# Optimization experiments

Hardware: AMD Instinct MI355X
Metric: run time of the kernel (lower is better)

Reference implementation:

```python
import jax, jax.numpy as jnp
import numpy as np

NUM_HEADS = 12
NUM_GROUPS = 4
LN_EPS = 1e-12
NEG = -10000.0


def _ln(x, g, b):
    m = x.mean(-1, keepdims=True)
    v = ((x - m) ** 2).mean(-1, keepdims=True)
    return (x - m) * jax.lax.rsqrt(v + LN_EPS) * g + b


def _attention(h, ext_mask, Wattn, battn, ln):
    # h: [B,S,H]; ext_mask additive [B,1,1,S]; Wattn [4,H,H] = (q,k,v,o); battn [4,H]; ln [2,H]
    B, S, H = h.shape
    dh = H // NUM_HEADS
    q = (h @ Wattn[0] + battn[0]).reshape(B, S, NUM_HEADS, dh)
    k = (h @ Wattn[1] + battn[1]).reshape(B, S, NUM_HEADS, dh)
    v = (h @ Wattn[2] + battn[2]).reshape(B, S, NUM_HEADS, dh)
    scores = jnp.einsum('bqhd,bkhd->bhqk', q, k) * (1.0 / np.sqrt(dh)) + ext_mask
    p = jax.nn.softmax(scores, axis=-1)
    ctx = jnp.einsum('bhqk,bkhd->bqhd', p, v).reshape(B, S, H)
    # BertSelfOutput: dense + residual + LayerNorm
    return _ln(ctx @ Wattn[3] + battn[3] + h, ln[0], ln[1])


def _ffn(x, Wi, bi, Wo, bo, ln):
    # BertIntermediate (gelu) + BertOutput (dense + residual + LayerNorm)
    return _ln(jax.nn.gelu(x @ Wi + bi, approximate=False) @ Wo + bo + x, ln[0], ln[1])


def _bert_layer(h, ext_mask, Wattn, battn, ln_attn, Wi, bi, Wo, bo, ln_out):
    a = _attention(h, ext_mask, Wattn, battn, ln_attn)
    return _ffn(a, Wi, bi, Wo, bo, ln_out)


def _hier_attention(h, hier_mask, Wattn, battn, ln_attn, Wi, bi, Wo, bo, ln_out):
    # group masks [G,B,S]: 1 where hier_mask == group_id (ids 1..G)
    gids = jnp.arange(1, NUM_GROUPS + 1)
    masks = (hier_mask[None] == gids[:, None, None]).astype(h.dtype)  # [G,B,S]
    ext = (1.0 - masks)[:, :, None, None, :] * NEG                    # [G,B,1,1,S]
    # one full BertLayer per group (vectorized over G instead of batch concat)
    outs = jax.vmap(lambda m: _bert_layer(h, m, Wattn, battn, ln_attn, Wi, bi, Wo, bo, ln_out))(ext)  # [G,B,S,H]
    return jnp.sum(outs * masks[..., None], axis=0)


def reference(hidden_states, attention_mask, main_Wattn, main_battn, main_ln_attn,
              main_Wi, main_bi, main_Wo, main_bo, main_ln_out,
              hier_Wattn, hier_battn, hier_ln_attn, hier_Wi, hier_bi, hier_Wo,
              hier_bo, hier_ln_out, hier_mask):
    attn_out = _attention(hidden_states, attention_mask, main_Wattn, main_battn, main_ln_attn)
    hier_out = _hier_attention(hidden_states, hier_mask, hier_Wattn, hier_battn,
                               hier_ln_attn, hier_Wi, hier_bi, hier_Wo, hier_bo, hier_ln_out)
    combined = attn_out + hier_out
    return _ffn(combined, main_Wi, main_bi, main_Wo, main_bo, main_ln_out)


def setup_inputs() -> dict:
    key = jax.random.key(0)
    ks = jax.random.split(key, 20)
    B, S, H, F = 8, 512, 768, 3072
    W = 0.02  # weight init scale

    def layer_params(k):
        kk = jax.random.split(k, 8)
        return dict(
            Wattn=jax.random.normal(kk[0], (4, H, H), jnp.float32) * W,
            battn=jax.random.normal(kk[1], (4, H), jnp.float32) * W,
            ln_attn=jnp.stack([1.0 + jax.random.normal(kk[2], (H,), jnp.float32) * W,
                               jax.random.normal(kk[3], (H,), jnp.float32) * W]),
            Wi=jax.random.normal(kk[4], (H, F), jnp.float32) * W,
            bi=jax.random.normal(kk[5], (F,), jnp.float32) * W,
            Wo=jax.random.normal(kk[6], (F, H), jnp.float32) * W,
            bo=jax.random.normal(kk[7], (H,), jnp.float32) * W,
            ln_out=jnp.stack([1.0 + jax.random.normal(kk[2], (H,), jnp.float32) * W,
                              jax.random.normal(kk[3], (H,), jnp.float32) * W]),
        )

    main = layer_params(ks[0])
    hier = layer_params(ks[1])
    inp = {
        'hidden_states': jax.random.normal(ks[2], (B, S, H), jnp.float32),
        'attention_mask': jnp.zeros((B, 1, 1, S), jnp.float32),
        'hier_mask': jax.random.randint(ks[3], (B, S), 0, 5).astype(jnp.int64),
    }
    for name, p in (('main', main), ('hier', hier)):
        for k2, v in p.items():
            inp[f'{name}_{k2}'] = v
    return inp
```

## Files before the change

kernel.cpp:

```cpp
#include <hip/hip_runtime.h>
#include <hip/hip_bf16.h>

#define DI __device__ __forceinline__

typedef __attribute__((ext_vector_type(4))) float  f32x4;
typedef __attribute__((ext_vector_type(8))) short  s16x8;
typedef __attribute__((ext_vector_type(4))) short  s16x4;
typedef __attribute__((ext_vector_type(8))) __bf16 bf16x8;

DI short f2bf(float f) {
  union { float f; unsigned u; } v; v.f = f;
  unsigned r = v.u + 0x7fffu + ((v.u >> 16) & 1u);
  return (short)(r >> 16);
}

DI f32x4 mfma16(s16x8 a, s16x8 b, f32x4 c) {
  return __builtin_amdgcn_mfma_f32_16x16x32_bf16(
      __builtin_bit_cast(bf16x8, a), __builtin_bit_cast(bf16x8, b), c, 0, 0, 0);
}

typedef const __attribute__((address_space(1))) unsigned* gas_p;
typedef __attribute__((address_space(3))) unsigned* las_p;
DI void gload16(const void* g, void* l) {
  __builtin_amdgcn_global_load_lds((gas_p)g, (las_p)l, 16, 0, 0);
}

__global__ __launch_bounds__(256) void cast_bf16(const float* __restrict__ x,
                                                 short* __restrict__ y) {
  const int i = (blockIdx.x * 256 + threadIdx.x) * 4;
  const float4 t = *(const float4*)&x[i];
  s16x4 o;
  o[0] = f2bf(t.x); o[1] = f2bf(t.y); o[2] = f2bf(t.z); o[3] = f2bf(t.w);
  *(s16x4*)&y[i] = o;
}

struct TJob { const float* src; short* dst; int K, N, tile0; };
struct TJobs { TJob j[12]; };

__global__ __launch_bounds__(256) void transpose_w(TJobs jobs) {
  __shared__ float T[32][33];
  const int t = blockIdx.x;
  int ji = 0;
#pragma unroll
  for (int i = 1; i < 12; ++i) if (jobs.j[i].tile0 <= t) ji = i;
  const float* src = jobs.j[ji].src;
  short* dst = jobs.j[ji].dst;
  const int K = jobs.j[ji].K, N = jobs.j[ji].N;
  const int lt = t - jobs.j[ji].tile0;
  const int tn = N >> 5;
  const int n0 = (lt % tn) << 5, k0 = (lt / tn) << 5;
  const int tid = threadIdx.x;
#pragma unroll
  for (int i = 0; i < 4; ++i) {
    const int c = i * 256 + tid, r = c >> 5, cc = c & 31;
    T[cc][r] = src[(long long)(k0 + r) * N + n0 + cc];
  }
  __syncthreads();
#pragma unroll
  for (int i = 0; i < 4; ++i) {
    const int c = i * 256 + tid, r = c >> 5, cc = c & 31;
    dst[(long long)(n0 + r) * K + k0 + cc] = f2bf(T[r][cc]);
  }
}

__global__ __launch_bounds__(256) void transpose_v(const short* __restrict__ QKV,
                                                   short* __restrict__ Vt) {
  __shared__ short T[64][72];
  const int bh = blockIdx.y;
  const int b = bh / 12, hh = bh % 12;
  const int s0 = blockIdx.x * 64;
  const int tid = threadIdx.x;
#pragma unroll
  for (int i = 0; i < 2; ++i) {
    const int c = i * 256 + tid;
    const int s = c >> 3, d = (c & 7) * 8;
    s16x8 v = *(const s16x8*)&QKV[(long long)(b * 512 + s0 + s) * 2304 + 1536 + hh * 64 + d];
    *(s16x8*)&T[s][d] = v;
  }
  __syncthreads();
#pragma unroll
  for (int i = 0; i < 2; ++i) {
    const int c = i * 256 + tid;
    const int d = c >> 3, s = (c & 7) * 8;
    s16x8 v;
#pragma unroll
    for (int j = 0; j < 8; ++j) v[j] = T[s + j][d];
    *(s16x8*)&Vt[(long long)bh * 32768 + (long long)d * 512 + s0 + s] = v;
  }
}

template<int BM, int BN, int WM, int WN, int EPI>
__global__ __launch_bounds__(256) void gemm_bt(
    const short* __restrict__ A, int lda, long long sA,
    const short* __restrict__ B, int ldb, long long sB,
    void* __restrict__ Cv, int ldc,
    long long cOuter, int cInner, int cStride,
    const float* __restrict__ bias,
    int K, int nSplit) {
  constexpr int BK = 32;
  constexpr int WNW = BN / WN;
  constexpr int MFR = WM / 16, NFR = WN / 16;
  constexpr int ACH = BM * 4;
  constexpr int BCH = BN * 4;

  __shared__ short As[BM * BK];
  __shared__ short Bs[BN * BK];

  const int z = blockIdx.z;
  const int zb = z / nSplit, zs = z - zb * nSplit;
  const short* Ab = A + (long long)zb * sA + (long long)zs * K;
  const short* Bb = B + (long long)zb * sB + (long long)zs * K;
  const long long cOff = (long long)(z / cInner) * cOuter + (long long)(z % cInner) * cStride;

  const int bm = blockIdx.x * BM;
  const int bn = blockIdx.y * BN;
  const int tid = threadIdx.x;
  const int wave = tid >> 6, lane = tid & 63;
  const int wm = (wave / WNW) * WM;
  const int wn = (wave % WNW) * WN;
  const int l16 = lane & 15, lk = lane >> 4;

  f32x4 acc[MFR][NFR] = {};

  for (int kt = 0; kt < K; kt += BK) {
    __syncthreads();
#pragma unroll
    for (int i = 0; i < ACH / 256; ++i) {
      const int c = i * 256 + tid;
      gload16(Ab + (long long)(bm + (c >> 2)) * lda + kt + (c & 3) * 8,
              &As[(i * 256 + wave * 64) * 8]);
    }
#pragma unroll
    for (int i = 0; i < BCH / 256; ++i) {
      const int c = i * 256 + tid;
      gload16(Bb + (long long)(bn + (c >> 2)) * ldb + kt + (c & 3) * 8,
              &Bs[(i * 256 + wave * 64) * 8]);
    }
    __syncthreads();
    s16x8 af[MFR], bfr[NFR];
#pragma unroll
    for (int mi = 0; mi < MFR; ++mi)
      af[mi] = *(const s16x8*)&As[(wm + mi * 16 + l16) * BK + lk * 8];
#pragma unroll
    for (int ni = 0; ni < NFR; ++ni)
      bfr[ni] = *(const s16x8*)&Bs[(wn + ni * 16 + l16) * BK + lk * 8];
#pragma unroll
    for (int mi = 0; mi < MFR; ++mi)
#pragma unroll
      for (int ni = 0; ni < NFR; ++ni)
        acc[mi][ni] = mfma16(af[mi], bfr[ni], acc[mi][ni]);
  }

#pragma unroll
  for (int ni = 0; ni < NFR; ++ni) {
    const int col = bn + wn + ni * 16 + l16;
    const float bv = (EPI != 2 && bias) ? bias[col] : 0.f;
#pragma unroll
    for (int mi = 0; mi < MFR; ++mi) {
#pragma unroll
      for (int r = 0; r < 4; ++r) {
        const int row = bm + wm + mi * 16 + lk * 4 + r;
        const long long idx = cOff + (long long)row * ldc + col;
        float v = acc[mi][ni][r] + bv;
        if constexpr (EPI == 0) {
          ((short*)Cv)[idx] = f2bf(v);
        } else if constexpr (EPI == 1) {
          v = 0.5f * v * (1.f + erff(v * 0.70710678118654752f));
          ((short*)Cv)[idx] = f2bf(v);
        } else {
          ((float*)Cv)[idx] = v;
        }
      }
    }
  }
}

template<int HIER>
__global__ __launch_bounds__(256) void attn_scores(
    const short* __restrict__ QKV,
    const float* __restrict__ amask,
    const int* __restrict__ hmask,
    short* __restrict__ P) {
  __shared__ short Qs[32 * 64];
  __shared__ short Ks[256 * 64];
  __shared__ float red[32 * 4];
  __shared__ int   hm[512];

  const int bh = blockIdx.y;
  const int b = bh / 12, hh = bh % 12;
  const int q0 = blockIdx.x * 32;
  const int tid = threadIdx.x;
  const int wave = tid >> 6, lane = tid & 63;
  const int l16 = lane & 15, lk = lane >> 4;
  const long long rowbase = (long long)(b * 512) * 2304 + hh * 64;

  {
    const int c = tid;
    gload16(QKV + rowbase + (long long)(q0 + (c >> 3)) * 2304 + (c & 7) * 8,
            &Qs[wave * 64 * 8]);
  }
  if constexpr (HIER) {
    for (int i = tid; i < 512; i += 256) hm[i] = hmask[b * 512 + i];
  }

  f32x4 acc[2][8] = {};
#pragma unroll
  for (int kc = 0; kc < 2; ++kc) {
    if (kc) __syncthreads();
#pragma unroll
    for (int i = 0; i < 8; ++i) {
      const int c = i * 256 + tid;
      gload16(QKV + rowbase + 768 + (long long)(kc * 256 + (c >> 3)) * 2304 + (c & 7) * 8,
              &Ks[(i * 256 + wave * 64) * 8]);
    }
    __syncthreads();
#pragma unroll
    for (int ks = 0; ks < 2; ++ks) {
      s16x8 af[2], bfr[4];
#pragma unroll
      for (int mi = 0; mi < 2; ++mi)
        af[mi] = *(const s16x8*)&Qs[(mi * 16 + l16) * 64 + ks * 32 + lk * 8];
#pragma unroll
      for (int ni = 0; ni < 4; ++ni)
        bfr[ni] = *(const s16x8*)&Ks[(wave * 64 + ni * 16 + l16) * 64 + ks * 32 + lk * 8];
#pragma unroll
      for (int mi = 0; mi < 2; ++mi)
#pragma unroll
        for (int ni = 0; ni < 4; ++ni)
          acc[mi][kc * 4 + ni] = mfma16(af[mi], bfr[ni], acc[mi][kc * 4 + ni]);
    }
  }

  int gq[2][4];
  if constexpr (HIER) {
#pragma unroll
    for (int mi = 0; mi < 2; ++mi)
#pragma unroll
      for (int r = 0; r < 4; ++r)
        gq[mi][r] = hm[q0 + mi * 16 + lk * 4 + r];
  }
  int hk[8]; float am[8];
#pragma unroll
  for (int nig = 0; nig < 8; ++nig) {
    const int col = (nig >> 2) * 256 + wave * 64 + (nig & 3) * 16 + l16;
    if constexpr (HIER) hk[nig] = hm[col];
    else                am[nig] = amask[b * 512 + col];
  }
#pragma unroll
  for (int mi = 0; mi < 2; ++mi)
#pragma unroll
    for (int nig = 0; nig < 8; ++nig)
#pragma unroll
      for (int r = 0; r < 4; ++r) {
        float v = acc[mi][nig][r] * 0.125f;
        if constexpr (HIER) v += (hk[nig] == gq[mi][r]) ? 0.f : -10000.f;
        else                v += am[nig];
        acc[mi][nig][r] = v;
      }

  float mx[2][4];
#pragma unroll
  for (int mi = 0; mi < 2; ++mi)
#pragma unroll
    for (int r = 0; r < 4; ++r) {
      float m = acc[mi][0][r];
#pragma unroll
      for (int nig = 1; nig < 8; ++nig) m = fmaxf(m, acc[mi][nig][r]);
#pragma unroll
      for (int d = 1; d < 16; d <<= 1) m = fmaxf(m, __shfl_xor(m, d));
      mx[mi][r] = m;
      red[(mi * 16 + lk * 4 + r) * 4 + wave] = m;
    }
  __syncthreads();
#pragma unroll
  for (int mi = 0; mi < 2; ++mi)
#pragma unroll
    for (int r = 0; r < 4; ++r) {
      const int q = mi * 16 + lk * 4 + r;
      mx[mi][r] = fmaxf(fmaxf(red[q * 4], red[q * 4 + 1]),
                        fmaxf(red[q * 4 + 2], red[q * 4 + 3]));
    }
  __syncthreads();

  float sm[2][4];
#pragma unroll
  for (int mi = 0; mi < 2; ++mi)
#pragma unroll
    for (int r = 0; r < 4; ++r) {
      float s = 0.f;
#pragma unroll
      for (int nig = 0; nig < 8; ++nig) {
        const float e = __expf(acc[mi][nig][r] - mx[mi][r]);
        acc[mi][nig][r] = e;
        s += e;
      }
#pragma unroll
      for (int d = 1; d < 16; d <<= 1) s += __shfl_xor(s, d);
      sm[mi][r] = s;
      red[(mi * 16 + lk * 4 + r) * 4 + wave] = s;
    }
  __syncthreads();
#pragma unroll
  for (int mi = 0; mi < 2; ++mi)
#pragma unroll
    for (int r = 0; r < 4; ++r) {
      const int q = mi * 16 + lk * 4 + r;
      sm[mi][r] = 1.f / (red[q * 4] + red[q * 4 + 1] + red[q * 4 + 2] + red[q * 4 + 3]);
    }

  const long long Pbase = (long long)bh * 512 * 512;
#pragma unroll
  for (int mi = 0; mi < 2; ++mi)
#pragma unroll
    for (int nig = 0; nig < 8; ++nig) {
      const int col = (nig >> 2) * 256 + wave * 64 + (nig & 3) * 16 + l16;
#pragma unroll
      for (int r = 0; r < 4; ++r) {
        const int q = mi * 16 + lk * 4 + r;
        P[Pbase + (long long)(q0 + q) * 512 + col] = f2bf(acc[mi][nig][r] * sm[mi][r]);
      }
    }
}

template<int NS, int MODE>
__global__ __launch_bounds__(256) void ln_red(
    const float* __restrict__ part, const float* __restrict__ bias,
    const float* __restrict__ res, const float* __restrict__ ln,
    float* __restrict__ outf, short* __restrict__ outb,
    const int* __restrict__ hmask) {
  constexpr long long SP = 4096LL * 768;
  const int row = blockIdx.x * 4 + (threadIdx.x >> 6);
  const int lane = threadIdx.x & 63;
  const long long rb = (long long)row * 768;
  float v[12];
  float s = 0.f;
#pragma unroll
  for (int i = 0; i < 3; ++i) {
    const int c4 = lane + (i << 6);
    float4 t = ((const float4*)(res + rb))[c4];
    const float4 bv = ((const float4*)bias)[c4];
    t.x += bv.x; t.y += bv.y; t.z += bv.z; t.w += bv.w;
#pragma unroll
    for (int ss = 0; ss < NS; ++ss) {
      const float4 p = ((const float4*)(part + ss * SP + rb))[c4];
      t.x += p.x; t.y += p.y; t.z += p.z; t.w += p.w;
    }
    v[i * 4 + 0] = t.x; v[i * 4 + 1] = t.y; v[i * 4 + 2] = t.z; v[i * 4 + 3] = t.w;
    s += t.x + t.y + t.z + t.w;
  }
#pragma unroll
  for (int d = 1; d < 64; d <<= 1) s += __shfl_xor(s, d);
  const float mean = s * (1.f / 768.f);
  float vs = 0.f;
#pragma unroll
  for (int i = 0; i < 12; ++i) { const float dv = v[i] - mean; vs += dv * dv; }
#pragma unroll
  for (int d = 1; d < 64; d <<= 1) vs += __shfl_xor(vs, d);
  const float rstd = rsqrtf(vs * (1.f / 768.f) + 1e-12f);
  int keep = 1;
  if constexpr (MODE == 2) keep = (hmask[row] != 0);
#pragma unroll
  for (int i = 0; i < 3; ++i) {
    const int c4 = lane + (i << 6);
    const float4 g = ((const float4*)ln)[c4];
    const float4 be = ((const float4*)(ln + 768))[c4];
    const float gg[4] = {g.x, g.y, g.z, g.w}, bb[4] = {be.x, be.y, be.z, be.w};
    float resv[4];
#pragma unroll
    for (int j = 0; j < 4; ++j) {
      float yv = (v[i * 4 + j] - mean) * rstd * gg[j] + bb[j];
      if constexpr (MODE == 2) {
        const float a = outf[rb + c4 * 4 + j];
        yv = a + (keep ? yv : 0.f);
      }
      resv[j] = yv;
    }
    float4 of; of.x = resv[0]; of.y = resv[1]; of.z = resv[2]; of.w = resv[3];
    ((float4*)(outf + rb))[c4] = of;
    if constexpr (MODE >= 1) {
      s16x4 ob;
#pragma unroll
      for (int j = 0; j < 4; ++j) ob[j] = f2bf(resv[j]);
      *(s16x4*)&outb[rb + c4 * 4] = ob;
    }
  }
}

extern "C" void kernel_launch(void* const* d_in, const int* in_sizes, int n_in,
                              void* d_out, int out_size, void* d_ws, size_t ws_size,
                              hipStream_t stream) {
  (void)in_sizes; (void)n_in; (void)out_size; (void)ws_size;
  const float* h      = (const float*)d_in[0];
  const float* amask  = (const float*)d_in[1];
  const int*   hmask  = (const int*)d_in[2];
  const float* mWattn = (const float*)d_in[3];
  const float* mbattn = (const float*)d_in[4];
  const float* mlnA   = (const float*)d_in[5];
  const float* mWi    = (const float*)d_in[6];
  const float* mbi    = (const float*)d_in[7];
  const float* mWo    = (const float*)d_in[8];
  const float* mbo    = (const float*)d_in[9];
  const float* mlnO   = (const float*)d_in[10];
  const float* hWattn = (const float*)d_in[11];
  const float* hbattn = (const float*)d_in[12];
  const float* hlnA   = (const float*)d_in[13];
  const float* hWi    = (const float*)d_in[14];
  const float* hbi    = (const float*)d_in[15];
  const float* hWo    = (const float*)d_in[16];
  const float* hbo    = (const float*)d_in[17];
  const float* hlnO   = (const float*)d_in[18];
  float* out = (float*)d_out;

  char* ws = (char*)d_ws;
  size_t off = 0;
  auto alloc = [&](size_t bytes) {
    void* p = ws + off;
    off += (bytes + 255) & ~(size_t)255;
    return p;
  };
  short* wq_m = (short*)alloc(2304ull * 768 * 2);
  short* wq_h = (short*)alloc(2304ull * 768 * 2);
  short* wo2  = (short*)alloc(2ull * 768 * 768 * 2);
  short* wi_m = (short*)alloc(3072ull * 768 * 2);
  short* wi_h = (short*)alloc(3072ull * 768 * 2);
  short* wf_m = (short*)alloc(768ull * 3072 * 2);
  short* wf_h = (short*)alloc(768ull * 3072 * 2);
  short* hbf  = (short*)alloc(4096ull * 768 * 2);
  short* qkv  = (short*)alloc(4096ull * 2304 * 2);
  short* vt   = (short*)alloc(96ull * 64 * 512 * 2);
  short* Pb   = (short*)alloc(96ull * 512 * 512 * 2);
  short* ctxb = (short*)alloc(2ull * 4096 * 768 * 2);
  float* pre1 = (float*)alloc(4096ull * 768 * 4);
  float* attn = (float*)alloc(4096ull * 768 * 4);
  short* abf  = (short*)alloc(4096ull * 768 * 2);
  short* cbf  = (short*)alloc(4096ull * 768 * 2);
  short* mid  = qkv;
  float* part = (float*)Pb;

  const long long SC = 4096LL * 768;

  cast_bf16<<<dim3(3072), dim3(256), 0, stream>>>(h, hbf);

  TJobs tj; int tile = 0; int nj = 0;
  auto add = [&](const float* s, short* d, int K, int N) {
    tj.j[nj].src = s; tj.j[nj].dst = d; tj.j[nj].K = K; tj.j[nj].N = N; tj.j[nj].tile0 = tile;
    tile += (K / 32) * (N / 32); nj++;
  };
  add(mWattn,              wq_m,              768, 768);
  add(mWattn + 589824,     wq_m + 589824,     768, 768);
  add(mWattn + 2 * 589824, wq_m + 2 * 589824, 768, 768);
  add(mWattn + 3 * 589824, wo2,               768, 768);
  add(mWi,                 wi_m,              768, 3072);
  add(mWo,                 wf_m,              3072, 768);
  add(hWattn,              wq_h,              768, 768);
  add(hWattn + 589824,     wq_h + 589824,     768, 768);
  add(hWattn + 2 * 589824, wq_h + 2 * 589824, 768, 768);
  add(hWattn + 3 * 589824, wo2 + 589824,      768, 768);
  add(hWi,                 wi_h,              768, 3072);
  add(hWo,                 wf_h,              3072, 768);
  transpose_w<<<dim3(tile), dim3(256), 0, stream>>>(tj);

  auto attn_path = [&](const short* wq, const float* battn, int hier, short* ctx) {
    gemm_bt<128, 128, 64, 64, 0><<<dim3(32, 18, 1), dim3(256), 0, stream>>>(
        hbf, 768, 0, wq, 768, 0, qkv, 2304, 0, 1, 0, battn, 768, 1);
    transpose_v<<<dim3(8, 96), dim3(256), 0, stream>>>(qkv, vt);
    if (hier)
      attn_scores<1><<<dim3(16, 96), dim3(256), 0, stream>>>(qkv, amask, hmask, Pb);
    else
      attn_scores<0><<<dim3(16, 96), dim3(256), 0, stream>>>(qkv, amask, hmask, Pb);
    gemm_bt<128, 64, 32, 64, 0><<<dim3(4, 1, 96), dim3(256), 0, stream>>>(
        Pb, 512, 262144LL, vt, 512, 32768LL,
        ctx, 768, 512LL * 768, 12, 64, nullptr, 512, 1);
  };

  attn_path(wq_m, mbattn, 0, ctxb);
  attn_path(wq_h, hbattn, 1, ctxb + SC);

  gemm_bt<128, 128, 64, 64, 2><<<dim3(32, 6, 4), dim3(256), 0, stream>>>(
      ctxb, 768, SC, wo2, 768, 589824LL, part, 768, SC, 1, 0, nullptr, 384, 2);
  ln_red<2, 0><<<dim3(1024), dim3(256), 0, stream>>>(
      part, mbattn + 2304, h, mlnA, attn, nullptr, nullptr);
  ln_red<2, 1><<<dim3(1024), dim3(256), 0, stream>>>(
      part + 2 * SC, hbattn + 2304, h, hlnA, pre1, abf, nullptr);

  gemm_bt<128, 128, 64, 64, 1><<<dim3(32, 24, 1), dim3(256), 0, stream>>>(
      abf, 768, 0, wi_h, 768, 0, mid, 3072, 0, 1, 0, hbi, 768, 1);
  gemm_bt<128, 128, 64, 64, 2><<<dim3(32, 6, 4), dim3(256), 0, stream>>>(
      mid, 3072, 0, wf_h, 3072, 0, part, 768, SC, 1, 0, nullptr, 768, 4);
  ln_red<4, 2><<<dim3(1024), dim3(256), 0, stream>>>(
      part, hbo, pre1, hlnO, attn, cbf, hmask);

  gemm_bt<128, 128, 64, 64, 1><<<dim3(32, 24, 1), dim3(256), 0, stream>>>(
      cbf, 768, 0, wi_m, 768, 0, mid, 3072, 0, 1, 0, mbi, 768, 1);
  gemm_bt<128, 128, 64, 64, 2><<<dim3(32, 6, 4), dim3(256), 0, stream>>>(
      mid, 3072, 0, wf_m, 3072, 0, part, 768, SC, 1, 0, nullptr, 768, 4);
  ln_red<4, 0><<<dim3(1024), dim3(256), 0, stream>>>(
      part, mbo, attn, mlnO, out, nullptr, nullptr);
}
```

Measured before the change: 386.6 us.

## Double-buffer GEMM LDS tiles and vectorize epilogue via transposed MFMA

```diff
diff --git a/kernel.cpp b/kernel.cpp
--- a/kernel.cpp
+++ b/kernel.cpp
@@ -103,8 +103,8 @@
   constexpr int ACH = BM * 4;
   constexpr int BCH = BN * 4;
 
-  __shared__ short As[BM * BK];
-  __shared__ short Bs[BN * BK];
+  __shared__ short As[2][BM * BK];
+  __shared__ short Bs[2][BN * BK];
 
   const int z = blockIdx.z;
   const int zb = z / nSplit, zs = z - zb * nSplit;
@@ -122,54 +122,67 @@
 
   f32x4 acc[MFR][NFR] = {};
 
-  for (int kt = 0; kt < K; kt += BK) {
-    __syncthreads();
+  auto stage = [&](int buf, int kt) {
 #pragma unroll
     for (int i = 0; i < ACH / 256; ++i) {
       const int c = i * 256 + tid;
       gload16(Ab + (long long)(bm + (c >> 2)) * lda + kt + (c & 3) * 8,
-              &As[(i * 256 + wave * 64) * 8]);
+              &As[buf][(i * 256 + wave * 64) * 8]);
     }
 #pragma unroll
     for (int i = 0; i < BCH / 256; ++i) {
       const int c = i * 256 + tid;
       gload16(Bb + (long long)(bn + (c >> 2)) * ldb + kt + (c & 3) * 8,
-              &Bs[(i * 256 + wave * 64) * 8]);
-    }
+              &Bs[buf][(i * 256 + wave * 64) * 8]);
+    }
+  };
+
+  stage(0, 0);
+  __syncthreads();
+  int cur = 0;
+  for (int kt = 0; kt < K; kt += BK) {
+    if (kt + BK < K) stage(cur ^ 1, kt + BK);
+    s16x8 af[MFR], bfr[NFR];
+#pragma unroll
+    for (int mi = 0; mi < MFR; ++mi)
+      af[mi] = *(const s16x8*)&As[cur][(wm + mi * 16 + l16) * BK + lk * 8];
+#pragma unroll
+    for (int ni = 0; ni < NFR; ++ni)
+      bfr[ni] = *(const s16x8*)&Bs[cur][(wn + ni * 16 + l16) * BK + lk * 8];
+#pragma unroll
+    for (int mi = 0; mi < MFR; ++mi)
+#pragma unroll
+      for (int ni = 0; ni < NFR; ++ni)
+        acc[mi][ni] = mfma16(bfr[ni], af[mi], acc[mi][ni]);
     __syncthreads();
-    s16x8 af[MFR], bfr[NFR];
-#pragma unroll
-    for (int mi = 0; mi < MFR; ++mi)
-      af[mi] = *(const s16x8*)&As[(wm + mi * 16 + l16) * BK + lk * 8];
-#pragma unroll
-    for (int ni = 0; ni < NFR; ++ni)
-      bfr[ni] = *(const s16x8*)&Bs[(wn + ni * 16 + l16) * BK + lk * 8];
-#pragma unroll
-    for (int mi = 0; mi < MFR; ++mi)
-#pragma unroll
-      for (int ni = 0; ni < NFR; ++ni)
-        acc[mi][ni] = mfma16(af[mi], bfr[ni], acc[mi][ni]);
-  }
-
-#pragma unroll
-  for (int ni = 0; ni < NFR; ++ni) {
-    const int col = bn + wn + ni * 16 + l16;
-    const float bv = (EPI != 2 && bias) ? bias[col] : 0.f;
-#pragma unroll
-    for (int mi = 0; mi < MFR; ++mi) {
-#pragma unroll
-      for (int r = 0; r < 4; ++r) {
-        const int row = bm + wm + mi * 16 + lk * 4 + r;
-        const long long idx = cOff + (long long)row * ldc + col;
-        float v = acc[mi][ni][r] + bv;
-        if constexpr (EPI == 0) {
-          ((short*)Cv)[idx] = f2bf(v);
-        } else if constexpr (EPI == 1) {
-          v = 0.5f * v * (1.f + erff(v * 0.70710678118654752f));
-          ((short*)Cv)[idx] = f2bf(v);
-        } else {
-          ((float*)Cv)[idx] = v;
+    cur ^= 1;
+  }
+
+#pragma unroll
+  for (int mi = 0; mi < MFR; ++mi) {
+    const int row = bm + wm + mi * 16 + l16;
+#pragma unroll
+    for (int ni = 0; ni < NFR; ++ni) {
+      const int col = bn + wn + ni * 16 + lk * 4;
+      const long long idx = cOff + (long long)row * ldc + col;
+      f32x4 bv = {};
+      if (EPI != 2 && bias) bv = *(const f32x4*)&bias[col];
+      f32x4 v = acc[mi][ni] + bv;
+      if constexpr (EPI == 0) {
+        s16x4 o;
+#pragma unroll
+        for (int r = 0; r < 4; ++r) o[r] = f2bf(v[r]);
+        *(s16x4*)&((short*)Cv)[idx] = o;
+      } else if constexpr (EPI == 1) {
+        s16x4 o;
+#pragma unroll
+        for (int r = 0; r < 4; ++r) {
+          const float g = 0.5f * v[r] * (1.f + erff(v[r] * 0.70710678118654752f));
+          o[r] = f2bf(g);
         }
+        *(s16x4*)&((short*)Cv)[idx] = o;
+      } else {
+        *(f32x4*)&((float*)Cv)[idx] = v;
       }
     }
   }
```

Measured after the change: 379.6 us. About the same (-1.8%).
